# Kernel tuning notes

Hardware: AMD Instinct MI355X
Metric: run time of the kernel (lower is better)

Reference implementation:

```python
import jax, jax.numpy as jnp
import numpy as np

# dims
T, INPUT_DIM = 128, 512
C_INT, ISQ, DIM, C = 8, 16, 256, 8  # internal_channels, input_square_dim, dim, n_channel
OSQ, OUT_CH = 8, 16                  # output_square_dim, output_size // osq^2
INPUT_SCALE, S1, S2 = 1.0, 0.9, 0.1
K1, D1, K2, D2 = 3, 1, 5, 2


def dw_circ_conv(x, w, dilation):
    """Depthwise conv with circular padding. x: [B,C,H,W], w: [C,1,k,k]."""
    k = w.shape[-1]
    pad = dilation * (k - 1) // 2
    xp = jnp.pad(x, ((0, 0), (0, 0), (pad, pad), (pad, pad)), mode='wrap')
    return jax.lax.conv_general_dilated(
        xp, w, window_strides=(1, 1), padding='VALID',
        rhs_dilation=(dilation, dilation), feature_group_count=x.shape[1])


def setup_inputs() -> dict:
    key = jax.random.key(0)
    ks = jax.random.split(key, 10)
    X = jax.random.normal(ks[0], (T, INPUT_DIM), jnp.float32)
    # nn.Linear weight [out, in]
    W_embed = jax.random.normal(ks[1], (C_INT * ISQ * ISQ, INPUT_DIM), jnp.float32) * 0.02
    mask_coarse = jax.random.bernoulli(ks[2], 0.5, (1, 1, ISQ, ISQ)).astype(jnp.float32)
    mask_fine = jax.random.bernoulli(ks[3], 0.5, (1, 1, DIM, DIM)).astype(jnp.float32)
    # ConvTranspose2d weight [in_ch, out_ch, k, k], k = dim // isq = 16
    W_deconv = jax.random.normal(ks[4], (C_INT, C, DIM // ISQ, DIM // ISQ), jnp.float32) * 0.02

    def lateral_w(k, ksz, p):
        # LateralConnections with conn_exp=1: |w| * bernoulli(p), normalized per output channel
        w = jnp.abs(jax.random.normal(k, (C, 1, ksz, ksz), jnp.float32))
        m = jax.random.bernoulli(jax.random.fold_in(k, 1), p, w.shape).astype(jnp.float32)
        w = w * m
        return w / w.sum(axis=(1, 2, 3), keepdims=True)

    w1 = lateral_w(ks[5], K1, 0.9)
    w2 = lateral_w(ks[6], K2, 0.9)
    # output Conv2d: [out_ch, in_ch, k, k], k = dim // osq = 32
    w_out = jax.random.normal(ks[7], (OUT_CH, C, DIM // OSQ, DIM // OSQ), jnp.float32) * 0.01
    b_out = jax.random.normal(ks[8], (OUT_CH,), jnp.float32) * 0.01
    return dict(X=X, W_embed=W_embed, mask_coarse=mask_coarse, mask_fine=mask_fine,
                W_deconv=W_deconv, w1=w1, w2=w2, w_out=w_out, b_out=b_out)


def reference(X, W_embed, mask_coarse, mask_fine, W_deconv, w1, w2, w_out, b_out):
    t = X.shape[0]
    ksz = W_deconv.shape[-1]
    # CorticalInput
    u = (X @ W_embed.T).reshape(t, C_INT, ISQ, ISQ) * mask_coarse  # [T,Cint,isq,isq]
    # ConvTranspose2d with stride == kernel_size (non-overlapping) == block expansion
    u = jnp.einsum('tcij,coab->toiajb', u, W_deconv).reshape(t, C, ISQ * ksz, ISQ * ksz)
    u = INPUT_SCALE * u * mask_fine  # [T,C,dim,dim]

    # sequential reservoir scan
    def step(Z, x):
        Z = jnp.tanh(S1 * dw_circ_conv(Z, w1, D1) + S2 * dw_circ_conv(Z, w2, D2) + x)
        return Z, Z[0]

    Z0 = jnp.zeros((1, C, DIM, DIM), X.dtype)
    _, outs = jax.lax.scan(step, Z0, u)  # outs: [T,C,dim,dim]

    # readout conv (kernel == stride == dim // osq)
    ko = w_out.shape[-1]
    y = jax.lax.conv_general_dilated(outs, w_out, (ko, ko), 'VALID')
    y = y + b_out[None, :, None, None]
    return y.reshape(t, -1)
```

## Files before the change

### kernel.cpp

```cpp
#include <hip/hip_runtime.h>
#include <math.h>

#define SB_OFF   0
#define E_OFF    524288

typedef float vf4 __attribute__((ext_vector_type(4)));

__device__ __forceinline__ float fast_tanh(float x) {
  x = fminf(fmaxf(x, -15.f), 15.f);
  float ex = __expf(2.f * x);
  return __fdividef(ex - 1.f, ex + 1.f);
}

template <int CTRL>
__device__ __forceinline__ float dpp_add(float v) {
  int x = __builtin_amdgcn_update_dpp(0, __float_as_int(v), CTRL, 0xF, 0xF, true);
  return v + __int_as_float(x);
}

__device__ __forceinline__ void st16(float* p, float a, float b, float c, float d) {
  vf4 v; v.x = a; v.y = b; v.z = c; v.w = d;
  asm volatile("global_store_dwordx4 %0, %1, off sc0 sc1" :: "v"(p), "v"(v) : "memory");
}
__device__ __forceinline__ vf4 ld16(const float* p) {
  vf4 r;
  asm volatile("global_load_dwordx4 %0, %1, off sc0 sc1\n"
               "s_waitcnt vmcnt(0)"
               : "=&v"(r) : "v"(p) : "memory");
  return r;
}
__device__ __forceinline__ void tag_store(unsigned* p, unsigned v) {
  asm volatile("s_waitcnt vmcnt(0)\n"
               "global_store_dword %0, %1, off sc0 sc1" :: "v"(p), "v"(v) : "memory");
}
__device__ __forceinline__ unsigned poll_tag(const unsigned* p) {
  unsigned v;
  asm volatile("global_load_dword %0, %1, off sc0 sc1\n"
               "s_waitcnt vmcnt(0)" : "=&v"(v) : "v"(p) : "memory");
  return v;
}

__global__ __launch_bounds__(256) void prep_kernel(
    const float* __restrict__ X, const float* __restrict__ W_embed,
    const float* __restrict__ mask_coarse, const float* __restrict__ b_out,
    float* __restrict__ ws, float* __restrict__ out)
{
  __shared__ float Xl[128][36];
  __shared__ float Wl[8][36];

  const int tid = threadIdx.x, bid = blockIdx.x;
  float* eb = ws + E_OFF;

  if (tid < 192) {
    ws[SB_OFF + bid * 1024 + 832 + tid] = 0.f;
    ws[SB_OFF + 262144 + bid * 1024 + 832 + tid] = 0.f;
  }

  {
    int idx = bid * 512 + tid * 2;
    out[idx]     = b_out[(idx >> 6) & 15];
    out[idx + 1] = b_out[((idx + 1) >> 6) & 15];
  }

  const int o0 = bid * 8;
  const int ol = tid & 7;
  const int tg = tid >> 3;
  float acc[4] = {0.f, 0.f, 0.f, 0.f};

  for (int k0 = 0; k0 < 512; k0 += 32) {
    __syncthreads();
#pragma unroll
    for (int p = 0; p < 4; ++p) {
      int tr = p * 32 + (tid >> 3);
      int kc = (tid & 7) * 4;
      *(float4*)&Xl[tr][kc] = *(const float4*)&X[(size_t)tr * 512 + k0 + kc];
    }
    if (tid < 64) {
      int wr = tid >> 3, wc = (tid & 7) * 4;
      *(float4*)&Wl[wr][wc] = *(const float4*)&W_embed[(size_t)(o0 + wr) * 512 + k0 + wc];
    }
    __syncthreads();
#pragma unroll
    for (int kk = 0; kk < 8; ++kk) {
      float4 w4 = *(const float4*)&Wl[ol][kk * 4];
#pragma unroll
      for (int i = 0; i < 4; ++i) {
        float4 x4 = *(const float4*)&Xl[tg * 4 + i][kk * 4];
        acc[i] = fmaf(w4.x, x4.x, fmaf(w4.y, x4.y, fmaf(w4.z, x4.z, fmaf(w4.w, x4.w, acc[i]))));
      }
    }
  }
  const int o = o0 + ol;
  float mc = mask_coarse[o & 255];
#pragma unroll
  for (int i = 0; i < 4; ++i)
    eb[(size_t)(tg * 4 + i) * 2048 + o] = acc[i] * mc;
}

__global__ __launch_bounds__(512, 2) void scan_kernel(
    const float* __restrict__ mask_fine, const float* __restrict__ W_deconv,
    const float* __restrict__ w1, const float* __restrict__ w2,
    const float* __restrict__ w_out, float* __restrict__ ws,
    float* __restrict__ out)
{
  __shared__ float zin[2][72 * 44];
  __shared__ float rowbuf[2][64 * 17];

  const int tid  = threadIdx.x;
  const int bid  = blockIdx.x;
  const int ch   = bid >> 5;
  const int tile = bid & 31;
  const int tI = tile >> 3, tJ = tile & 7;
  const int r0 = tI << 6, c0 = tJ << 5;
  const int row = tid >> 3;
  const int cg  = tid & 7;
  const int lc  = cg << 2;

  float* Zb = ws + SB_OFF;
  const float* eb = ws + E_OFF;
  const int myoff = (ch * 32 + tile) << 10;

  const int i0 = (r0 + row) >> 4;
  const int jj = (c0 + lc) >> 4;
  float4 wd[8];
#pragma unroll
  for (int c = 0; c < 8; ++c)
    wd[c] = *(const float4*)&W_deconv[(((c * 8 + ch) * 16) + (row & 15)) * 16 + (lc & 15)];
  float4 mf = *(const float4*)&mask_fine[(size_t)(r0 + row) * 256 + c0 + lc];
  float4 wo[16];
#pragma unroll
  for (int oc = 0; oc < 16; ++oc)
    wo[oc] = *(const float4*)&w_out[(((oc * 8 + ch) * 32) + (row & 31)) * 32 + lc];
  float w1s[9], w2s[25];
#pragma unroll
  for (int k = 0; k < 9; ++k)
    w1s[k] = __uint_as_float(__builtin_amdgcn_readfirstlane(__float_as_uint(w1[ch * 9 + k])));
#pragma unroll
  for (int k = 0; k < 25; ++k)
    w2s[k] = __uint_as_float(__builtin_amdgcn_readfirstlane(__float_as_uint(w2[ch * 25 + k])));

  int rd_src = 0, rd_dst = 0, rd_tag = 0;
  const bool hasrd = (tid < 208);
  if (hasrd) {
    int u = tid, di = 0, dj = 0, src = 0, dst = 0, wv = 0;
    if (u < 32) {
      di = -1; src = 128 + (u >> 3) * 32 + (u & 7) * 4;
      dst = (u >> 3) * 44 + 4 + (u & 7) * 4; wv = 7;
    } else if (u < 64) {
      int v = u - 32; di = 1; src = (v >> 3) * 32 + (v & 7) * 4;
      dst = (68 + (v >> 3)) * 44 + 4 + (v & 7) * 4; wv = 0;
    } else if (u < 128) {
      int v = u - 64; dj = -1; src = 512 + v * 4; dst = (4 + v) * 44; wv = v >> 3;
    } else if (u < 192) {
      int v = u - 128; dj = 1; src = 256 + v * 4; dst = (4 + v) * 44 + 36; wv = v >> 3;
    } else {
      int v = u - 192, c = v >> 2, r = v & 3;
      if (c == 0)      { di = -1; dj = -1; src = 816 + r * 4; dst = r * 44;            wv = 7; }
      else if (c == 1) { di = -1; dj = 1;  src = 800 + r * 4; dst = r * 44 + 36;       wv = 7; }
      else if (c == 2) { di = 1;  dj = -1; src = 784 + r * 4; dst = (68 + r) * 44;     wv = 0; }
      else             { di = 1;  dj = 1;  src = 768 + r * 4; dst = (68 + r) * 44 + 36; wv = 0; }
    }
    int nI = (tI + di) & 3, nJ = (tJ + dj) & 7;
    int roff = (ch * 32 + nI * 8 + nJ) << 10;
    rd_src = roff + src;
    rd_tag = roff + 832 + wv * 16;
    rd_dst = dst;
  }

  for (int k = tid; k < 2 * 72 * 44; k += 512) zin[0][k] = 0.f;
  __syncthreads();

  float ev[8];
#pragma unroll
  for (int c = 0; c < 8; ++c)
    ev[c] = eb[c * 256 + i0 * 16 + jj];

  for (int t = 0; t < 128; ++t) {
    float* sb = Zb + (size_t)((t + 1) & 1) * 262144;
    const float* zr = zin[t & 1];
    float*       zw = zin[(t + 1) & 1];
    float*       rb = rowbuf[t & 1];

    float c1a[4] = {0, 0, 0, 0}, c2a[4] = {0, 0, 0, 0};
    {
      float w[12];
      auto load_row = [&](int zrr) {
        float4 A  = *(const float4*)&zr[zrr * 44 + lc];
        float4 B  = *(const float4*)&zr[zrr * 44 + lc + 4];
        float4 Cq = *(const float4*)&zr[zrr * 44 + lc + 8];
        w[0]=A.x; w[1]=A.y; w[2]=A.z; w[3]=A.w;
        w[4]=B.x; w[5]=B.y; w[6]=B.z; w[7]=B.w;
        w[8]=Cq.x; w[9]=Cq.y; w[10]=Cq.z; w[11]=Cq.w;
      };
      auto k2row = [&](int a) {
#pragma unroll
        for (int j = 0; j < 4; ++j)
#pragma unroll
          for (int b = 0; b < 5; ++b)
            c2a[j] = fmaf(w[j + 2 * b], w2s[a * 5 + b], c2a[j]);
      };
      auto k1row = [&](int a) {
#pragma unroll
        for (int j = 0; j < 4; ++j)
#pragma unroll
          for (int b = 0; b < 3; ++b)
            c1a[j] = fmaf(w[j + 3 + b], w1s[a * 3 + b], c1a[j]);
      };
      load_row(row + 0); k2row(0);
      load_row(row + 2); k2row(1);
      load_row(row + 3); k1row(0);
      load_row(row + 4); k1row(1); k2row(2);
      load_row(row + 5); k1row(2);
      load_row(row + 6); k2row(3);
      load_row(row + 8); k2row(4);
    }
    float zv[4];
    {
      const float* mfp = (const float*)&mf;
#pragma unroll
      for (int j = 0; j < 4; ++j) {
        float u = 0.f;
#pragma unroll
        for (int c = 0; c < 8; ++c)
          u = fmaf(ev[c], ((const float*)&wd[c])[j], u);
        float val = fmaf(0.9f, c1a[j], fmaf(0.1f, c2a[j], mfp[j] * u));
        zv[j] = fast_tanh(val);
      }
    }

    if (t < 127) {
      float* rec = sb + myoff;
      if (row < 4)   st16(rec + row * 32 + lc, zv[0], zv[1], zv[2], zv[3]);
      if (row >= 60) st16(rec + 128 + (row - 60) * 32 + lc, zv[0], zv[1], zv[2], zv[3]);
      if (lc == 0)   st16(rec + 256 + row * 4, zv[0], zv[1], zv[2], zv[3]);
      if (lc == 28)  st16(rec + 512 + row * 4, zv[0], zv[1], zv[2], zv[3]);
      if (row < 4 && lc == 0)   st16(rec + 768 + row * 4, zv[0], zv[1], zv[2], zv[3]);
      if (row < 4 && lc == 28)  st16(rec + 784 + row * 4, zv[0], zv[1], zv[2], zv[3]);
      if (row >= 60 && lc == 0) st16(rec + 800 + (row - 60) * 4, zv[0], zv[1], zv[2], zv[3]);
      if (row >= 60 && lc == 28) st16(rec + 816 + (row - 60) * 4, zv[0], zv[1], zv[2], zv[3]);
    }

    *(float4*)&zw[(4 + row) * 44 + 4 + lc] = make_float4(zv[0], zv[1], zv[2], zv[3]);

    float racc[16];
#pragma unroll
    for (int oc = 0; oc < 16; ++oc) {
      const float* wop = (const float*)&wo[oc];
      racc[oc] = fmaf(zv[0], wop[0], fmaf(zv[1], wop[1], fmaf(zv[2], wop[2], zv[3] * wop[3])));
    }
#pragma unroll
    for (int k = 0; k < 16; ++k) {
      racc[k] = dpp_add<0xB1>(racc[k]);
      racc[k] = dpp_add<0x4E>(racc[k]);
      racc[k] = dpp_add<0x141>(racc[k]);
    }
    rb[row * 17 + (cg << 1)]     = racc[cg << 1];
    rb[row * 17 + (cg << 1) + 1] = racc[(cg << 1) + 1];

    if (t < 127 && (tid & 63) == 0)
      tag_store((unsigned*)(sb + myoff + 832 + (tid >> 6) * 16), (unsigned)(t + 1));

    float evn[8];
    if (t < 127) {
#pragma unroll
      for (int c = 0; c < 8; ++c)
        evn[c] = eb[(size_t)(t + 1) * 2048 + c * 256 + i0 * 16 + jj];
    }

    if (t < 127 && hasrd) {
      const unsigned tg = (unsigned)(t + 1);
      const unsigned* ta = (const unsigned*)(sb + rd_tag);
      int spins = 0;
      while (poll_tag(ta) != tg) {
        __builtin_amdgcn_s_sleep(1);
        if (++spins > (1 << 18)) break;
      }
      vf4 v = ld16(sb + rd_src);
      zw[rd_dst]     = v.x;
      zw[rd_dst + 1] = v.y;
      zw[rd_dst + 2] = v.z;
      zw[rd_dst + 3] = v.w;
    }

    __syncthreads();

    if (tid < 32) {
      int p = tid >> 4, oc = tid & 15;
      float s = 0.f;
#pragma unroll
      for (int r = 0; r < 32; ++r) s += rb[(p * 32 + r) * 17 + oc];
      atomicAdd(&out[t * 1024 + oc * 64 + (2 * tI + p) * 8 + tJ], s);
    }

    if (t < 127) {
#pragma unroll
      for (int c = 0; c < 8; ++c) ev[c] = evn[c];
    }
  }
}

extern "C" void kernel_launch(void* const* d_in, const int* in_sizes, int n_in,
                              void* d_out, int out_size, void* d_ws, size_t ws_size,
                              hipStream_t stream) {
  const float* X           = (const float*)d_in[0];
  const float* W_embed     = (const float*)d_in[1];
  const float* mask_coarse = (const float*)d_in[2];
  const float* mask_fine   = (const float*)d_in[3];
  const float* W_deconv    = (const float*)d_in[4];
  const float* w1          = (const float*)d_in[5];
  const float* w2          = (const float*)d_in[6];
  const float* w_out       = (const float*)d_in[7];
  const float* b_out       = (const float*)d_in[8];
  float* ws  = (float*)d_ws;
  float* out = (float*)d_out;

  prep_kernel<<<dim3(256), dim3(256), 0, stream>>>(X, W_embed, mask_coarse, b_out, ws, out);
  scan_kernel<<<dim3(256), dim3(512), 0, stream>>>(mask_fine, W_deconv, w1, w2, w_out, ws, out);
}
```

Measured before the change: 549.4 us.

## Warp-specialize scan block into conv and readout/halo-exchange thread groups

Doubles the block to 1024 threads and splits it into two roles. The first 512 threads compute the stencil, tanh and halo stores. The other 512 run the readout for the previous step from shared memory, then spin on neighbour tags and gather the halo. This takes the readout reduction and the halo polling off the critical path of the conv threads, so readout is pipelined one step behind. In exchange it raises register and occupancy pressure under launch_bounds(1024,1), and it adds a final epilogue for the last timestep.

```diff
diff --git a/kernel.cpp b/kernel.cpp
--- a/kernel.cpp
+++ b/kernel.cpp
@@ -97,7 +97,7 @@
     eb[(size_t)(tg * 4 + i) * 2048 + o] = acc[i] * mc;
 }
 
-__global__ __launch_bounds__(512, 2) void scan_kernel(
+__global__ __launch_bounds__(1024, 1) void scan_kernel(
     const float* __restrict__ mask_fine, const float* __restrict__ W_deconv,
     const float* __restrict__ w1, const float* __restrict__ w2,
     const float* __restrict__ w_out, float* __restrict__ ws,
@@ -112,8 +112,10 @@
   const int tile = bid & 31;
   const int tI = tile >> 3, tJ = tile & 7;
   const int r0 = tI << 6, c0 = tJ << 5;
-  const int row = tid >> 3;
-  const int cg  = tid & 7;
+  const bool isconv = (tid < 512);
+  const int lt  = tid & 511;
+  const int row = lt >> 3;
+  const int cg  = lt & 7;
   const int lc  = cg << 2;
 
   float* Zb = ws + SB_OFF;
@@ -123,57 +125,58 @@
   const int i0 = (r0 + row) >> 4;
   const int jj = (c0 + lc) >> 4;
   float4 wd[8];
-#pragma unroll
-  for (int c = 0; c < 8; ++c)
-    wd[c] = *(const float4*)&W_deconv[(((c * 8 + ch) * 16) + (row & 15)) * 16 + (lc & 15)];
-  float4 mf = *(const float4*)&mask_fine[(size_t)(r0 + row) * 256 + c0 + lc];
+  float4 mf = make_float4(0.f, 0.f, 0.f, 0.f);
+  float w1s[9], w2s[25];
+  if (isconv) {
+#pragma unroll
+    for (int c = 0; c < 8; ++c)
+      wd[c] = *(const float4*)&W_deconv[(((c * 8 + ch) * 16) + (row & 15)) * 16 + (lc & 15)];
+    mf = *(const float4*)&mask_fine[(size_t)(r0 + row) * 256 + c0 + lc];
+#pragma unroll
+    for (int k = 0; k < 9; ++k)
+      w1s[k] = __uint_as_float(__builtin_amdgcn_readfirstlane(__float_as_uint(w1[ch * 9 + k])));
+#pragma unroll
+    for (int k = 0; k < 25; ++k)
+      w2s[k] = __uint_as_float(__builtin_amdgcn_readfirstlane(__float_as_uint(w2[ch * 25 + k])));
+  }
+
   float4 wo[16];
-#pragma unroll
-  for (int oc = 0; oc < 16; ++oc)
-    wo[oc] = *(const float4*)&w_out[(((oc * 8 + ch) * 32) + (row & 31)) * 32 + lc];
-  float w1s[9], w2s[25];
-#pragma unroll
-  for (int k = 0; k < 9; ++k)
-    w1s[k] = __uint_as_float(__builtin_amdgcn_readfirstlane(__float_as_uint(w1[ch * 9 + k])));
-#pragma unroll
-  for (int k = 0; k < 25; ++k)
-    w2s[k] = __uint_as_float(__builtin_amdgcn_readfirstlane(__float_as_uint(w2[ch * 25 + k])));
-
   int rd_src = 0, rd_dst = 0, rd_tag = 0;
-  const bool hasrd = (tid < 208);
-  if (hasrd) {
-    int u = tid, di = 0, dj = 0, src = 0, dst = 0, wv = 0;
-    if (u < 32) {
-      di = -1; src = 128 + (u >> 3) * 32 + (u & 7) * 4;
-      dst = (u >> 3) * 44 + 4 + (u & 7) * 4; wv = 7;
-    } else if (u < 64) {
-      int v = u - 32; di = 1; src = (v >> 3) * 32 + (v & 7) * 4;
-      dst = (68 + (v >> 3)) * 44 + 4 + (v & 7) * 4; wv = 0;
-    } else if (u < 128) {
-      int v = u - 64; dj = -1; src = 512 + v * 4; dst = (4 + v) * 44; wv = v >> 3;
-    } else if (u < 192) {
-      int v = u - 128; dj = 1; src = 256 + v * 4; dst = (4 + v) * 44 + 36; wv = v >> 3;
-    } else {
-      int v = u - 192, c = v >> 2, r = v & 3;
-      if (c == 0)      { di = -1; dj = -1; src = 816 + r * 4; dst = r * 44;            wv = 7; }
-      else if (c == 1) { di = -1; dj = 1;  src = 800 + r * 4; dst = r * 44 + 36;       wv = 7; }
-      else if (c == 2) { di = 1;  dj = -1; src = 784 + r * 4; dst = (68 + r) * 44;     wv = 0; }
-      else             { di = 1;  dj = 1;  src = 768 + r * 4; dst = (68 + r) * 44 + 36; wv = 0; }
-    }
-    int nI = (tI + di) & 3, nJ = (tJ + dj) & 7;
-    int roff = (ch * 32 + nI * 8 + nJ) << 10;
-    rd_src = roff + src;
-    rd_tag = roff + 832 + wv * 16;
-    rd_dst = dst;
-  }
-
-  for (int k = tid; k < 2 * 72 * 44; k += 512) zin[0][k] = 0.f;
+  bool hasrd = false;
+  if (!isconv) {
+#pragma unroll
+    for (int oc = 0; oc < 16; ++oc)
+      wo[oc] = *(const float4*)&w_out[(((oc * 8 + ch) * 32) + (row & 31)) * 32 + lc];
+    hasrd = (lt < 208);
+    if (hasrd) {
+      int u = lt, di = 0, dj = 0, src = 0, dst = 0, wv = 0;
+      if (u < 32) {
+        di = -1; src = 128 + (u >> 3) * 32 + (u & 7) * 4;
+        dst = (u >> 3) * 44 + 4 + (u & 7) * 4; wv = 7;
+      } else if (u < 64) {
+        int v = u - 32; di = 1; src = (v >> 3) * 32 + (v & 7) * 4;
+        dst = (68 + (v >> 3)) * 44 + 4 + (v & 7) * 4; wv = 0;
+      } else if (u < 128) {
+        int v = u - 64; dj = -1; src = 512 + v * 4; dst = (4 + v) * 44; wv = v >> 3;
+      } else if (u < 192) {
+        int v = u - 128; dj = 1; src = 256 + v * 4; dst = (4 + v) * 44 + 36; wv = v >> 3;
+      } else {
+        int v = u - 192, c = v >> 2, r = v & 3;
+        if (c == 0)      { di = -1; dj = -1; src = 816 + r * 4; dst = r * 44;            wv = 7; }
+        else if (c == 1) { di = -1; dj = 1;  src = 800 + r * 4; dst = r * 44 + 36;       wv = 7; }
+        else if (c == 2) { di = 1;  dj = -1; src = 784 + r * 4; dst = (68 + r) * 44;     wv = 0; }
+        else             { di = 1;  dj = 1;  src = 768 + r * 4; dst = (68 + r) * 44 + 36; wv = 0; }
+      }
+      int nI = (tI + di) & 3, nJ = (tJ + dj) & 7;
+      int roff = (ch * 32 + nI * 8 + nJ) << 10;
+      rd_src = roff + src;
+      rd_tag = roff + 832 + wv * 16;
+      rd_dst = dst;
+    }
+  }
+
+  for (int k = tid; k < 2 * 72 * 44; k += 1024) zin[0][k] = 0.f;
   __syncthreads();
-
-  float ev[8];
-#pragma unroll
-  for (int c = 0; c < 8; ++c)
-    ev[c] = eb[c * 256 + i0 * 16 + jj];
 
   for (int t = 0; t < 128; ++t) {
     float* sb = Zb + (size_t)((t + 1) & 1) * 262144;
@@ -181,72 +184,128 @@
     float*       zw = zin[(t + 1) & 1];
     float*       rb = rowbuf[t & 1];
 
-    float c1a[4] = {0, 0, 0, 0}, c2a[4] = {0, 0, 0, 0};
-    {
-      float w[12];
-      auto load_row = [&](int zrr) {
-        float4 A  = *(const float4*)&zr[zrr * 44 + lc];
-        float4 B  = *(const float4*)&zr[zrr * 44 + lc + 4];
-        float4 Cq = *(const float4*)&zr[zrr * 44 + lc + 8];
-        w[0]=A.x; w[1]=A.y; w[2]=A.z; w[3]=A.w;
-        w[4]=B.x; w[5]=B.y; w[6]=B.z; w[7]=B.w;
-        w[8]=Cq.x; w[9]=Cq.y; w[10]=Cq.z; w[11]=Cq.w;
-      };
-      auto k2row = [&](int a) {
-#pragma unroll
-        for (int j = 0; j < 4; ++j)
-#pragma unroll
-          for (int b = 0; b < 5; ++b)
-            c2a[j] = fmaf(w[j + 2 * b], w2s[a * 5 + b], c2a[j]);
-      };
-      auto k1row = [&](int a) {
-#pragma unroll
-        for (int j = 0; j < 4; ++j)
-#pragma unroll
-          for (int b = 0; b < 3; ++b)
-            c1a[j] = fmaf(w[j + 3 + b], w1s[a * 3 + b], c1a[j]);
-      };
-      load_row(row + 0); k2row(0);
-      load_row(row + 2); k2row(1);
-      load_row(row + 3); k1row(0);
-      load_row(row + 4); k1row(1); k2row(2);
-      load_row(row + 5); k1row(2);
-      load_row(row + 6); k2row(3);
-      load_row(row + 8); k2row(4);
-    }
-    float zv[4];
-    {
-      const float* mfp = (const float*)&mf;
-#pragma unroll
-      for (int j = 0; j < 4; ++j) {
-        float u = 0.f;
-#pragma unroll
-        for (int c = 0; c < 8; ++c)
-          u = fmaf(ev[c], ((const float*)&wd[c])[j], u);
-        float val = fmaf(0.9f, c1a[j], fmaf(0.1f, c2a[j], mfp[j] * u));
-        zv[j] = fast_tanh(val);
-      }
-    }
-
-    if (t < 127) {
-      float* rec = sb + myoff;
-      if (row < 4)   st16(rec + row * 32 + lc, zv[0], zv[1], zv[2], zv[3]);
-      if (row >= 60) st16(rec + 128 + (row - 60) * 32 + lc, zv[0], zv[1], zv[2], zv[3]);
-      if (lc == 0)   st16(rec + 256 + row * 4, zv[0], zv[1], zv[2], zv[3]);
-      if (lc == 28)  st16(rec + 512 + row * 4, zv[0], zv[1], zv[2], zv[3]);
-      if (row < 4 && lc == 0)   st16(rec + 768 + row * 4, zv[0], zv[1], zv[2], zv[3]);
-      if (row < 4 && lc == 28)  st16(rec + 784 + row * 4, zv[0], zv[1], zv[2], zv[3]);
-      if (row >= 60 && lc == 0) st16(rec + 800 + (row - 60) * 4, zv[0], zv[1], zv[2], zv[3]);
-      if (row >= 60 && lc == 28) st16(rec + 816 + (row - 60) * 4, zv[0], zv[1], zv[2], zv[3]);
-    }
-
-    *(float4*)&zw[(4 + row) * 44 + 4 + lc] = make_float4(zv[0], zv[1], zv[2], zv[3]);
-
+    if (isconv) {
+      float ev[8];
+#pragma unroll
+      for (int c = 0; c < 8; ++c)
+        ev[c] = eb[(size_t)t * 2048 + c * 256 + i0 * 16 + jj];
+
+      float c1a[4] = {0, 0, 0, 0}, c2a[4] = {0, 0, 0, 0};
+      {
+        float w[12];
+        auto load_row = [&](int zrr) {
+          float4 A  = *(const float4*)&zr[zrr * 44 + lc];
+          float4 B  = *(const float4*)&zr[zrr * 44 + lc + 4];
+          float4 Cq = *(const float4*)&zr[zrr * 44 + lc + 8];
+          w[0]=A.x; w[1]=A.y; w[2]=A.z; w[3]=A.w;
+          w[4]=B.x; w[5]=B.y; w[6]=B.z; w[7]=B.w;
+          w[8]=Cq.x; w[9]=Cq.y; w[10]=Cq.z; w[11]=Cq.w;
+        };
+        auto k2row = [&](int a) {
+#pragma unroll
+          for (int j = 0; j < 4; ++j)
+#pragma unroll
+            for (int b = 0; b < 5; ++b)
+              c2a[j] = fmaf(w[j + 2 * b], w2s[a * 5 + b], c2a[j]);
+        };
+        auto k1row = [&](int a) {
+#pragma unroll
+          for (int j = 0; j < 4; ++j)
+#pragma unroll
+            for (int b = 0; b < 3; ++b)
+              c1a[j] = fmaf(w[j + 3 + b], w1s[a * 3 + b], c1a[j]);
+        };
+        load_row(row + 0); k2row(0);
+        load_row(row + 2); k2row(1);
+        load_row(row + 3); k1row(0);
+        load_row(row + 4); k1row(1); k2row(2);
+        load_row(row + 5); k1row(2);
+        load_row(row + 6); k2row(3);
+        load_row(row + 8); k2row(4);
+      }
+      float zv[4];
+      {
+        const float* mfp = (const float*)&mf;
+#pragma unroll
+        for (int j = 0; j < 4; ++j) {
+          float u = 0.f;
+#pragma unroll
+          for (int c = 0; c < 8; ++c)
+            u = fmaf(ev[c], ((const float*)&wd[c])[j], u);
+          float val = fmaf(0.9f, c1a[j], fmaf(0.1f, c2a[j], mfp[j] * u));
+          zv[j] = fast_tanh(val);
+        }
+      }
+
+      if (t < 127) {
+        float* rec = sb + myoff;
+        if (row < 4)   st16(rec + row * 32 + lc, zv[0], zv[1], zv[2], zv[3]);
+        if (row >= 60) st16(rec + 128 + (row - 60) * 32 + lc, zv[0], zv[1], zv[2], zv[3]);
+        if (lc == 0)   st16(rec + 256 + row * 4, zv[0], zv[1], zv[2], zv[3]);
+        if (lc == 28)  st16(rec + 512 + row * 4, zv[0], zv[1], zv[2], zv[3]);
+        if (row < 4 && lc == 0)   st16(rec + 768 + row * 4, zv[0], zv[1], zv[2], zv[3]);
+        if (row < 4 && lc == 28)  st16(rec + 784 + row * 4, zv[0], zv[1], zv[2], zv[3]);
+        if (row >= 60 && lc == 0) st16(rec + 800 + (row - 60) * 4, zv[0], zv[1], zv[2], zv[3]);
+        if (row >= 60 && lc == 28) st16(rec + 816 + (row - 60) * 4, zv[0], zv[1], zv[2], zv[3]);
+        if ((lt & 63) == 0)
+          tag_store((unsigned*)(rec + 832 + (lt >> 6) * 16), (unsigned)(t + 1));
+      }
+
+      *(float4*)&zw[(4 + row) * 44 + 4 + lc] = make_float4(zv[0], zv[1], zv[2], zv[3]);
+    } else {
+      if (t >= 1) {
+        float4 z4 = *(const float4*)&zr[(4 + row) * 44 + 4 + lc];
+        float racc[16];
+#pragma unroll
+        for (int oc = 0; oc < 16; ++oc) {
+          const float* wop = (const float*)&wo[oc];
+          racc[oc] = fmaf(z4.x, wop[0], fmaf(z4.y, wop[1], fmaf(z4.z, wop[2], z4.w * wop[3])));
+        }
+#pragma unroll
+        for (int k = 0; k < 16; ++k) {
+          racc[k] = dpp_add<0xB1>(racc[k]);
+          racc[k] = dpp_add<0x4E>(racc[k]);
+          racc[k] = dpp_add<0x141>(racc[k]);
+        }
+        rb[row * 17 + (cg << 1)]     = racc[cg << 1];
+        rb[row * 17 + (cg << 1) + 1] = racc[(cg << 1) + 1];
+      }
+
+      if (t < 127 && hasrd) {
+        const unsigned tg = (unsigned)(t + 1);
+        const unsigned* ta = (const unsigned*)(sb + rd_tag);
+        int spins = 0;
+        while (poll_tag(ta) != tg) {
+          __builtin_amdgcn_s_sleep(1);
+          if (++spins > (1 << 18)) break;
+        }
+        vf4 v = ld16(sb + rd_src);
+        zw[rd_dst]     = v.x;
+        zw[rd_dst + 1] = v.y;
+        zw[rd_dst + 2] = v.z;
+        zw[rd_dst + 3] = v.w;
+      }
+    }
+
+    __syncthreads();
+
+    if (!isconv && lt < 32 && t >= 1) {
+      int p = lt >> 4, oc = lt & 15;
+      float s = 0.f;
+#pragma unroll
+      for (int r = 0; r < 32; ++r) s += rb[(p * 32 + r) * 17 + oc];
+      atomicAdd(&out[(t - 1) * 1024 + oc * 64 + (2 * tI + p) * 8 + tJ], s);
+    }
+  }
+
+  if (!isconv) {
+    const float* zf = zin[0];
+    float4 z4 = *(const float4*)&zf[(4 + row) * 44 + 4 + lc];
     float racc[16];
 #pragma unroll
     for (int oc = 0; oc < 16; ++oc) {
       const float* wop = (const float*)&wo[oc];
-      racc[oc] = fmaf(zv[0], wop[0], fmaf(zv[1], wop[1], fmaf(zv[2], wop[2], zv[3] * wop[3])));
+      racc[oc] = fmaf(z4.x, wop[0], fmaf(z4.y, wop[1], fmaf(z4.z, wop[2], z4.w * wop[3])));
     }
 #pragma unroll
     for (int k = 0; k < 16; ++k) {
@@ -254,48 +313,16 @@
       racc[k] = dpp_add<0x4E>(racc[k]);
       racc[k] = dpp_add<0x141>(racc[k]);
     }
-    rb[row * 17 + (cg << 1)]     = racc[cg << 1];
-    rb[row * 17 + (cg << 1) + 1] = racc[(cg << 1) + 1];
-
-    if (t < 127 && (tid & 63) == 0)
-      tag_store((unsigned*)(sb + myoff + 832 + (tid >> 6) * 16), (unsigned)(t + 1));
-
-    float evn[8];
-    if (t < 127) {
-#pragma unroll
-      for (int c = 0; c < 8; ++c)
-        evn[c] = eb[(size_t)(t + 1) * 2048 + c * 256 + i0 * 16 + jj];
-    }
-
-    if (t < 127 && hasrd) {
-      const unsigned tg = (unsigned)(t + 1);
-      const unsigned* ta = (const unsigned*)(sb + rd_tag);
-      int spins = 0;
-      while (poll_tag(ta) != tg) {
-        __builtin_amdgcn_s_sleep(1);
-        if (++spins > (1 << 18)) break;
-      }
-      vf4 v = ld16(sb + rd_src);
-      zw[rd_dst]     = v.x;
-      zw[rd_dst + 1] = v.y;
-      zw[rd_dst + 2] = v.z;
-      zw[rd_dst + 3] = v.w;
-    }
-
-    __syncthreads();
-
-    if (tid < 32) {
-      int p = tid >> 4, oc = tid & 15;
-      float s = 0.f;
-#pragma unroll
-      for (int r = 0; r < 32; ++r) s += rb[(p * 32 + r) * 17 + oc];
-      atomicAdd(&out[t * 1024 + oc * 64 + (2 * tI + p) * 8 + tJ], s);
-    }
-
-    if (t < 127) {
-#pragma unroll
-      for (int c = 0; c < 8; ++c) ev[c] = evn[c];
-    }
+    rowbuf[0][row * 17 + (cg << 1)]     = racc[cg << 1];
+    rowbuf[0][row * 17 + (cg << 1) + 1] = racc[(cg << 1) + 1];
+  }
+  __syncthreads();
+  if (!isconv && lt < 32) {
+    int p = lt >> 4, oc = lt & 15;
+    float s = 0.f;
+#pragma unroll
+    for (int r = 0; r < 32; ++r) s += rowbuf[0][(p * 32 + r) * 17 + oc];
+    atomicAdd(&out[127 * 1024 + oc * 64 + (2 * tI + p) * 8 + tJ], s);
   }
 }
 
@@ -315,5 +342,5 @@
   float* out = (float*)d_out;
 
   prep_kernel<<<dim3(256), dim3(256), 0, stream>>>(X, W_embed, mask_coarse, b_out, ws, out);
-  scan_kernel<<<dim3(256), dim3(512), 0, stream>>>(mask_fine, W_deconv, w1, w2, w_out, ws, out);
-}
+  scan_kernel<<<dim3(256), dim3(1024), 0, stream>>>(mask_fine, W_deconv, w1, w2, w_out, ws, out);
+}
```

Result: slower. 745.9 us (+35.8%).
